# Performance work log

Hardware: AMD Instinct MI355X
Metric: run time of the kernel (lower is better)

## Reference

```python
import jax, jax.numpy as jnp
import numpy as np

HIDDEN_DIM = 2048
NUM_HEADS = 16
HEAD_DIM = HIDDEN_DIM // NUM_HEADS
BATCH = 2
SEQ = 2048


def setup_inputs() -> dict:
    key = jax.random.key(0)
    ks = jax.random.split(key, 5)
    scale = 1.0 / np.sqrt(HIDDEN_DIM)
    x = jax.random.normal(ks[0], (BATCH, SEQ, HIDDEN_DIM), dtype=jnp.float32)
    w_q = jax.random.normal(ks[1], (HIDDEN_DIM, HIDDEN_DIM), dtype=jnp.float32) * scale
    w_k = jax.random.normal(ks[2], (HIDDEN_DIM, HIDDEN_DIM), dtype=jnp.float32) * scale
    w_v = jax.random.normal(ks[3], (HIDDEN_DIM, HIDDEN_DIM), dtype=jnp.float32) * scale
    w_o = jax.random.normal(ks[4], (HIDDEN_DIM, HIDDEN_DIM), dtype=jnp.float32) * scale
    return {"x": x, "w_q": w_q, "w_k": w_k, "w_v": w_v, "w_o": w_o}


def reference(x, w_q, w_k, w_v, w_o):
    # Projections: x @ W.T  (weights stored as (out, in) like torch)
    q = jnp.einsum('bsd,ed->bse', x, w_q)
    k = jnp.einsum('bsd,ed->bse', x, w_k)
    v = jnp.einsum('bsd,ed->bse', x, w_v)
    b, s, _ = q.shape
    # split heads: (b, h, s, hd)
    q = q.reshape(b, s, NUM_HEADS, HEAD_DIM).transpose(0, 2, 1, 3)
    k = k.reshape(b, s, NUM_HEADS, HEAD_DIM).transpose(0, 2, 1, 3)
    v = v.reshape(b, s, NUM_HEADS, HEAD_DIM).transpose(0, 2, 1, 3)
    scale = 1.0 / np.sqrt(HEAD_DIM)
    # Online-softmax tiling in the source (causal=False default) is
    # mathematically identical to standard softmax attention.
    scores = jnp.einsum('bhqd,bhkd->bhqk', q, k) * scale
    p = jax.nn.softmax(scores, axis=-1)
    o = jnp.einsum('bhqk,bhkd->bhqd', p, v)
    o = o.transpose(0, 2, 1, 3).reshape(b, s, HIDDEN_DIM)
    return jnp.einsum('bsd,ed->bse', o, w_o)
```

## Files before the change

kernel.cpp:

```cpp
#include <hip/hip_runtime.h>


typedef _Float16 half8 __attribute__((ext_vector_type(8)));
typedef float floatx4 __attribute__((ext_vector_type(4)));

__device__ __forceinline__ void async16(const void* g, void* l) {
  __builtin_amdgcn_global_load_lds((__attribute__((address_space(1))) void*)(g),
                                   (__attribute__((address_space(3))) void*)(l),
                                   16, 0, 0);
}

__global__ void cvt_f32_f16(const float* __restrict__ src, _Float16* __restrict__ dst,
                            int n4) {
  int i = blockIdx.x * blockDim.x + threadIdx.x;
  if (i >= n4) return;
  float4 v = reinterpret_cast<const float4*>(src)[i];
  union { _Float16 h[4]; short4 s; } u;
  u.h[0] = (_Float16)v.x; u.h[1] = (_Float16)v.y;
  u.h[2] = (_Float16)v.z; u.h[3] = (_Float16)v.w;
  reinterpret_cast<short4*>(dst)[i] = u.s;
}

__global__ void cvt_w4(const float* __restrict__ w0, const float* __restrict__ w1,
                       const float* __restrict__ w2, const float* __restrict__ w3,
                       _Float16* __restrict__ dst, float scale0) {
  int i = blockIdx.x * blockDim.x + threadIdx.x;
  int m = i >> 20, j = i & ((1 << 20) - 1);
  const float* src = (m == 0) ? w0 : (m == 1) ? w1 : (m == 2) ? w2 : w3;
  float sc = (m == 0) ? scale0 : 1.0f;
  float4 v = reinterpret_cast<const float4*>(src)[j];
  union { _Float16 h[4]; short4 s; } u;
  u.h[0] = (_Float16)(v.x * sc); u.h[1] = (_Float16)(v.y * sc);
  u.h[2] = (_Float16)(v.z * sc); u.h[3] = (_Float16)(v.w * sc);
  reinterpret_cast<short4*>(dst)[i] = u.s;
}

template <int OUT_MODE, int BM, int BN, int MINW>
__global__ __launch_bounds__(256, MINW)
void gemm_nt(const _Float16* __restrict__ A, const _Float16* __restrict__ Bw,
             void* __restrict__ Cv, void* __restrict__ Cv2, int K) {
  constexpr int MT = BM / 32;
  constexpr int NT = BN / 32;
  __shared__ _Float16 As[BM * 64];
  __shared__ _Float16 Bs[BN * 64];
  const int tid = threadIdx.x;
  const int wave = tid >> 6, lane = tid & 63;
  const int wm = wave >> 1, wn = wave & 1;
  const int l15 = lane & 15, l4 = lane >> 4;
  const int bm = blockIdx.y, bn = blockIdx.x;

  floatx4 acc[MT][NT] = {};

  for (int k0 = 0; k0 < K; k0 += 64) {
    __syncthreads();
#pragma unroll
    for (int i = 0; i < BM * 8 / 256; ++i) {
      int c = i * 256 + tid;
      int row = c >> 3, cc = c & 7;
      int g = cc ^ (row & 7);
      async16(A + (size_t)(bm * BM + row) * K + k0 + g * 8, &As[c * 8]);
    }
#pragma unroll
    for (int i = 0; i < BN * 8 / 256; ++i) {
      int c = i * 256 + tid;
      int row = c >> 3, cc = c & 7;
      int g = cc ^ (row & 7);
      async16(Bw + (size_t)(bn * BN + row) * K + k0 + g * 8, &Bs[c * 8]);
    }
    __syncthreads();
#pragma unroll
    for (int ks = 0; ks < 2; ++ks) {
      half8 af[MT], bf[NT];
      int ch = (ks * 4 + l4) ^ (l15 & 7);
#pragma unroll
      for (int t = 0; t < MT; ++t)
        af[t] = *reinterpret_cast<const half8*>(&As[(wm * (BM / 2) + t * 16 + l15) * 64 + ch * 8]);
#pragma unroll
      for (int t = 0; t < NT; ++t)
        bf[t] = *reinterpret_cast<const half8*>(&Bs[(wn * (BN / 2) + t * 16 + l15) * 64 + ch * 8]);
#pragma unroll
      for (int mt = 0; mt < MT; ++mt)
#pragma unroll
        for (int nt = 0; nt < NT; ++nt)
          acc[mt][nt] = __builtin_amdgcn_mfma_f32_16x16x32_f16(af[mt], bf[nt], acc[mt][nt], 0, 0, 0);
    }
  }

  const int rbase = bm * BM + wm * (BM / 2);
  const int cbase = bn * BN + wn * (BN / 2);
  if constexpr (OUT_MODE == 0) {
    if (cbase < 4096) {
      _Float16* C = (_Float16*)Cv + (size_t)(cbase >> 11) * (4096ull * 2048);
#pragma unroll
      for (int mt = 0; mt < MT; ++mt)
#pragma unroll
        for (int nt = 0; nt < NT; ++nt) {
          int r0 = rbase + mt * 16 + l4 * 4;
          int cg = (cbase + nt * 16 + l15) & 2047;
#pragma unroll
          for (int r = 0; r < 4; ++r)
            C[(size_t)(r0 + r) * 2048 + cg] = (_Float16)acc[mt][nt][r];
        }
    } else {
      _Float16* C = (_Float16*)Cv2;
#pragma unroll
      for (int mt = 0; mt < MT; ++mt)
#pragma unroll
        for (int nt = 0; nt < NT; ++nt) {
          int m0 = rbase + mt * 16 + l4 * 4;
          int d = cbase + nt * 16 + l15 - 4096;
          size_t base = (size_t)(m0 >> 11) * (2048ull * 2048) + (size_t)d * 2048 + (m0 & 2047);
          union { _Float16 h[4]; short4 s; } u;
#pragma unroll
          for (int r = 0; r < 4; ++r) u.h[r] = (_Float16)acc[mt][nt][r];
          *reinterpret_cast<short4*>(C + base) = u.s;
        }
    }
  } else {
    float* C = (float*)Cv;
#pragma unroll
    for (int mt = 0; mt < MT; ++mt)
#pragma unroll
      for (int nt = 0; nt < NT; ++nt) {
        int r0 = rbase + mt * 16 + l4 * 4;
        int cg = cbase + nt * 16 + l15;
#pragma unroll
        for (int r = 0; r < 4; ++r)
          C[(size_t)(r0 + r) * 2048 + cg] = acc[mt][nt][r];
      }
  }
}

__global__ __launch_bounds__(256, 2)
void flash_attn(const _Float16* __restrict__ Q, const _Float16* __restrict__ Kg,
                const _Float16* __restrict__ Vt, _Float16* __restrict__ O) {
  __shared__ _Float16 Ks[64 * 128];
  __shared__ _Float16 Vs[128 * 64];
  __shared__ _Float16 Ps[128 * 64];
  const int tid = threadIdx.x, wave = tid >> 6, lane = tid & 63;
  const int l15 = lane & 15, l4 = lane >> 4;
  const int bh = blockIdx.y, b = bh >> 4, h = bh & 15;
  const int q0 = blockIdx.x * 128;

  const _Float16* Qp = Q + ((size_t)(b * 2048 + q0 + wave * 32)) * 2048 + h * 128;
  const _Float16* Kp = Kg + (size_t)b * 2048 * 2048 + h * 128;
  const _Float16* Vp = Vt + (size_t)b * 2048 * 2048 + (size_t)(h * 128) * 2048;

  half8 qf[2][4];
#pragma unroll
  for (int mt = 0; mt < 2; ++mt)
#pragma unroll
    for (int ks = 0; ks < 4; ++ks)
      qf[mt][ks] = *reinterpret_cast<const half8*>(
          Qp + (size_t)(mt * 16 + l15) * 2048 + ks * 32 + l4 * 8);

  floatx4 oacc[2][8] = {};
  float lsum[2][4] = {};

  for (int k0 = 0; k0 < 2048; k0 += 64) {
    __syncthreads();
#pragma unroll
    for (int i = 0; i < 4; ++i) {
      int c = i * 256 + tid;
      int row = c >> 4, cc = c & 15;
      int g = cc ^ (row & 15);
      async16(Kp + (size_t)(k0 + row) * 2048 + g * 8, &Ks[c * 8]);
    }
#pragma unroll
    for (int i = 0; i < 4; ++i) {
      int c = i * 256 + tid;
      int row = c >> 3, cc = c & 7;
      int g = cc ^ (row & 7);
      async16(Vp + (size_t)row * 2048 + k0 + g * 8, &Vs[c * 8]);
    }
    __syncthreads();

    floatx4 sacc[2][4] = {};
#pragma unroll
    for (int ks = 0; ks < 4; ++ks) {
      half8 bf[4];
#pragma unroll
      for (int nt = 0; nt < 4; ++nt) {
        int row = nt * 16 + l15;
        int ch = (ks * 4 + l4) ^ l15;
        bf[nt] = *reinterpret_cast<const half8*>(&Ks[row * 128 + ch * 8]);
      }
#pragma unroll
      for (int mt = 0; mt < 2; ++mt)
#pragma unroll
        for (int nt = 0; nt < 4; ++nt)
          sacc[mt][nt] = __builtin_amdgcn_mfma_f32_16x16x32_f16(qf[mt][ks], bf[nt], sacc[mt][nt], 0, 0, 0);
    }

#pragma unroll
    for (int mt = 0; mt < 2; ++mt)
#pragma unroll
      for (int nt = 0; nt < 4; ++nt)
#pragma unroll
        for (int r = 0; r < 4; ++r) {
          float p = exp2f(sacc[mt][nt][r]);
          lsum[mt][r] += p;
          int rl = l4 * 4 + r;
          int ch = (nt * 2 + (l15 >> 3)) ^ (rl & 7);
          Ps[(wave * 32 + mt * 16 + rl) * 64 + ch * 8 + (l15 & 7)] = (_Float16)p;
        }

    __builtin_amdgcn_s_waitcnt(0xC07F);

#pragma unroll
    for (int ks2 = 0; ks2 < 2; ++ks2) {
      half8 pf[2];
#pragma unroll
      for (int mt = 0; mt < 2; ++mt)
        pf[mt] = *reinterpret_cast<const half8*>(
            &Ps[(wave * 32 + mt * 16 + l15) * 64 + (((ks2 * 4 + l4) ^ (l15 & 7)) * 8)]);
#pragma unroll
      for (int nt2 = 0; nt2 < 8; ++nt2) {
        int row = nt2 * 16 + l15;
        int ch = (ks2 * 4 + l4) ^ (row & 7);
        half8 vf = *reinterpret_cast<const half8*>(&Vs[row * 64 + ch * 8]);
#pragma unroll
        for (int mt = 0; mt < 2; ++mt)
          oacc[mt][nt2] = __builtin_amdgcn_mfma_f32_16x16x32_f16(pf[mt], vf, oacc[mt][nt2], 0, 0, 0);
      }
    }
  }

#pragma unroll
  for (int mt = 0; mt < 2; ++mt)
#pragma unroll
    for (int r = 0; r < 4; ++r) {
#pragma unroll
      for (int off = 1; off < 16; off <<= 1) lsum[mt][r] += __shfl_xor(lsum[mt][r], off);
    }

  _Float16* Op = O + ((size_t)(b * 2048 + q0 + wave * 32)) * 2048 + h * 128;
#pragma unroll
  for (int mt = 0; mt < 2; ++mt)
#pragma unroll
    for (int r = 0; r < 4; ++r) {
      float inv = 1.0f / lsum[mt][r];
#pragma unroll
      for (int nt2 = 0; nt2 < 8; ++nt2) {
        int row = mt * 16 + l4 * 4 + r;
        int col = nt2 * 16 + l15;
        Op[(size_t)row * 2048 + col] = (_Float16)(oacc[mt][nt2][r] * inv);
      }
    }
}

extern "C" void kernel_launch(void* const* d_in, const int* in_sizes, int n_in,
                              void* d_out, int out_size, void* d_ws, size_t ws_size,
                              hipStream_t stream) {
  const float* x = (const float*)d_in[0];
  const float* wq = (const float*)d_in[1];
  const float* wk = (const float*)d_in[2];
  const float* wv = (const float*)d_in[3];
  const float* wo = (const float*)d_in[4];
  float* out = (float*)d_out;

  const size_t XN = (size_t)4096 * 2048;
  const size_t WN = (size_t)2048 * 2048;
  _Float16* xh = (_Float16*)d_ws;
  _Float16* qh = xh + XN;
  _Float16* vth = xh + 3 * XN;
  _Float16* oh = xh + 4 * XN;
  _Float16* wqh = xh + 5 * XN;

  const float SM_SCALE = 0.08838834764831845f * 1.4426950408889634f;

  cvt_f32_f16<<<dim3((int)(XN / 4 / 256)), 256, 0, stream>>>(x, xh, (int)(XN / 4));
  cvt_w4<<<dim3((int)(4 * WN / 4 / 256)), 256, 0, stream>>>(wq, wk, wv, wo, wqh, SM_SCALE);

  gemm_nt<0, 128, 128, 1><<<dim3(48, 32), 256, 0, stream>>>(xh, wqh, qh, vth, 2048);
  flash_attn<<<dim3(16, 32), 256, 0, stream>>>(qh, qh + XN, vth, oh);
  gemm_nt<2, 128, 64, 4><<<dim3(32, 32), 256, 0, stream>>>(oh, wqh + 3 * WN, out, nullptr, 2048);
}
```

Before: 406.2 us.

## Split-K the output projection with a reduction pass and fuse conversion kernels

The output projection GEMM switches from 128x64 tiles over the full K to 128x128 tiles with split-K of two. Each half writes fp32 partials into the workspace, where the earlier intermediates are now dead, and a new reduce_add kernel sums the two halves into the output. The two fp32-to-fp16 conversion kernels are merged into one launch, and the GEMM template is fixed to 128x128 tiles. The aim is a bigger per-wave MFMA tile and one fewer launch, at the cost of writing and re-reading large fp32 partial buffers plus an extra kernel launch.

```diff
diff --git a/kernel.cpp b/kernel.cpp
--- a/kernel.cpp
+++ b/kernel.cpp
@@ -10,91 +10,84 @@
                                    16, 0, 0);
 }
 
-__global__ void cvt_f32_f16(const float* __restrict__ src, _Float16* __restrict__ dst,
-                            int n4) {
+__global__ void cvt_all(const float* __restrict__ x, const float* __restrict__ w0,
+                        const float* __restrict__ w1, const float* __restrict__ w2,
+                        const float* __restrict__ w3, _Float16* __restrict__ xh,
+                        _Float16* __restrict__ wh, float scale0) {
   int i = blockIdx.x * blockDim.x + threadIdx.x;
-  if (i >= n4) return;
-  float4 v = reinterpret_cast<const float4*>(src)[i];
-  union { _Float16 h[4]; short4 s; } u;
-  u.h[0] = (_Float16)v.x; u.h[1] = (_Float16)v.y;
-  u.h[2] = (_Float16)v.z; u.h[3] = (_Float16)v.w;
-  reinterpret_cast<short4*>(dst)[i] = u.s;
-}
-
-__global__ void cvt_w4(const float* __restrict__ w0, const float* __restrict__ w1,
-                       const float* __restrict__ w2, const float* __restrict__ w3,
-                       _Float16* __restrict__ dst, float scale0) {
-  int i = blockIdx.x * blockDim.x + threadIdx.x;
-  int m = i >> 20, j = i & ((1 << 20) - 1);
-  const float* src = (m == 0) ? w0 : (m == 1) ? w1 : (m == 2) ? w2 : w3;
-  float sc = (m == 0) ? scale0 : 1.0f;
-  float4 v = reinterpret_cast<const float4*>(src)[j];
+  const int XQ = 1 << 21;
+  float sc = 1.0f;
+  const float* src;
+  _Float16* dst;
+  int j;
+  if (i < XQ) { src = x; dst = xh; j = i; }
+  else {
+    int t = i - XQ;
+    int m = t >> 20;
+    src = (m == 0) ? w0 : (m == 1) ? w1 : (m == 2) ? w2 : w3;
+    if (m == 0) sc = scale0;
+    dst = wh; j = t;
+  }
+  int js = (i < XQ) ? j : (j & ((1 << 20) - 1));
+  float4 v = reinterpret_cast<const float4*>(src)[js];
   union { _Float16 h[4]; short4 s; } u;
   u.h[0] = (_Float16)(v.x * sc); u.h[1] = (_Float16)(v.y * sc);
   u.h[2] = (_Float16)(v.z * sc); u.h[3] = (_Float16)(v.w * sc);
-  reinterpret_cast<short4*>(dst)[i] = u.s;
-}
-
-template <int OUT_MODE, int BM, int BN, int MINW>
-__global__ __launch_bounds__(256, MINW)
+  reinterpret_cast<short4*>(dst)[j] = u.s;
+}
+
+template <int OUT_MODE>
+__global__ __launch_bounds__(256)
 void gemm_nt(const _Float16* __restrict__ A, const _Float16* __restrict__ Bw,
-             void* __restrict__ Cv, void* __restrict__ Cv2, int K) {
-  constexpr int MT = BM / 32;
-  constexpr int NT = BN / 32;
-  __shared__ _Float16 As[BM * 64];
-  __shared__ _Float16 Bs[BN * 64];
+             void* __restrict__ Cv, void* __restrict__ Cv2, int kLen) {
+  __shared__ _Float16 As[128 * 64];
+  __shared__ _Float16 Bs[128 * 64];
   const int tid = threadIdx.x;
   const int wave = tid >> 6, lane = tid & 63;
   const int wm = wave >> 1, wn = wave & 1;
   const int l15 = lane & 15, l4 = lane >> 4;
   const int bm = blockIdx.y, bn = blockIdx.x;
-
-  floatx4 acc[MT][NT] = {};
-
-  for (int k0 = 0; k0 < K; k0 += 64) {
-    __syncthreads();
-#pragma unroll
-    for (int i = 0; i < BM * 8 / 256; ++i) {
+  const int kStart = (OUT_MODE == 2) ? blockIdx.z * kLen : 0;
+
+  floatx4 acc[4][4] = {};
+
+  for (int k0 = kStart; k0 < kStart + kLen; k0 += 64) {
+    __syncthreads();
+#pragma unroll
+    for (int i = 0; i < 4; ++i) {
       int c = i * 256 + tid;
       int row = c >> 3, cc = c & 7;
       int g = cc ^ (row & 7);
-      async16(A + (size_t)(bm * BM + row) * K + k0 + g * 8, &As[c * 8]);
-    }
-#pragma unroll
-    for (int i = 0; i < BN * 8 / 256; ++i) {
-      int c = i * 256 + tid;
-      int row = c >> 3, cc = c & 7;
-      int g = cc ^ (row & 7);
-      async16(Bw + (size_t)(bn * BN + row) * K + k0 + g * 8, &Bs[c * 8]);
+      async16(A + (size_t)(bm * 128 + row) * 2048 + k0 + g * 8, &As[c * 8]);
+      async16(Bw + (size_t)(bn * 128 + row) * 2048 + k0 + g * 8, &Bs[c * 8]);
     }
     __syncthreads();
 #pragma unroll
     for (int ks = 0; ks < 2; ++ks) {
-      half8 af[MT], bf[NT];
+      half8 af[4], bf[4];
       int ch = (ks * 4 + l4) ^ (l15 & 7);
 #pragma unroll
-      for (int t = 0; t < MT; ++t)
-        af[t] = *reinterpret_cast<const half8*>(&As[(wm * (BM / 2) + t * 16 + l15) * 64 + ch * 8]);
-#pragma unroll
-      for (int t = 0; t < NT; ++t)
-        bf[t] = *reinterpret_cast<const half8*>(&Bs[(wn * (BN / 2) + t * 16 + l15) * 64 + ch * 8]);
-#pragma unroll
-      for (int mt = 0; mt < MT; ++mt)
-#pragma unroll
-        for (int nt = 0; nt < NT; ++nt)
+      for (int t = 0; t < 4; ++t) {
+        af[t] = *reinterpret_cast<const half8*>(&As[(wm * 64 + t * 16 + l15) * 64 + ch * 8]);
+        bf[t] = *reinterpret_cast<const half8*>(&Bs[(wn * 64 + t * 16 + l15) * 64 + ch * 8]);
+      }
+#pragma unroll
+      for (int mt = 0; mt < 4; ++mt)
+#pragma unroll
+        for (int nt = 0; nt < 4; ++nt)
           acc[mt][nt] = __builtin_amdgcn_mfma_f32_16x16x32_f16(af[mt], bf[nt], acc[mt][nt], 0, 0, 0);
     }
   }
 
-  const int rbase = bm * BM + wm * (BM / 2);
-  const int cbase = bn * BN + wn * (BN / 2);
+  const int rbase = bm * 128 + wm * 64;
+  const int cbase = bn * 128 + wn * 64;
   if constexpr (OUT_MODE == 0) {
     if (cbase < 4096) {
       _Float16* C = (_Float16*)Cv + (size_t)(cbase >> 11) * (4096ull * 2048);
 #pragma unroll
-      for (int mt = 0; mt < MT; ++mt)
-#pragma unroll
-        for (int nt = 0; nt < NT; ++nt) {
+      for (int mt = 0; mt < 4; ++mt)
+#pragma unroll
+        for (int nt = 0; nt < 4; ++nt) {
           int r0 = rbase + mt * 16 + l4 * 4;
           int cg = (cbase + nt * 16 + l15) & 2047;
 #pragma unroll
@@ -104,9 +97,9 @@
     } else {
       _Float16* C = (_Float16*)Cv2;
 #pragma unroll
-      for (int mt = 0; mt < MT; ++mt)
-#pragma unroll
-        for (int nt = 0; nt < NT; ++nt) {
+      for (int mt = 0; mt < 4; ++mt)
+#pragma unroll
+        for (int nt = 0; nt < 4; ++nt) {
           int m0 = rbase + mt * 16 + l4 * 4;
           int d = cbase + nt * 16 + l15 - 4096;
           size_t base = (size_t)(m0 >> 11) * (2048ull * 2048) + (size_t)d * 2048 + (m0 & 2047);
@@ -117,11 +110,11 @@
         }
     }
   } else {
-    float* C = (float*)Cv;
-#pragma unroll
-    for (int mt = 0; mt < MT; ++mt)
-#pragma unroll
-      for (int nt = 0; nt < NT; ++nt) {
+    float* C = (float*)Cv + (size_t)blockIdx.z * 8388608ull;
+#pragma unroll
+    for (int mt = 0; mt < 4; ++mt)
+#pragma unroll
+      for (int nt = 0; nt < 4; ++nt) {
         int r0 = rbase + mt * 16 + l4 * 4;
         int cg = cbase + nt * 16 + l15;
 #pragma unroll
@@ -129,6 +122,14 @@
           C[(size_t)(r0 + r) * 2048 + cg] = acc[mt][nt][r];
       }
   }
+}
+
+__global__ void reduce_add(const float* __restrict__ p, float* __restrict__ out) {
+  int i = blockIdx.x * blockDim.x + threadIdx.x;
+  float4 a = reinterpret_cast<const float4*>(p)[i];
+  float4 b = reinterpret_cast<const float4*>(p + 8388608)[i];
+  float4 o; o.x = a.x + b.x; o.y = a.y + b.y; o.z = a.z + b.z; o.w = a.w + b.w;
+  reinterpret_cast<float4*>(out)[i] = o;
 }
 
 __global__ __launch_bounds__(256, 2)
@@ -266,13 +267,13 @@
   _Float16* vth = xh + 3 * XN;
   _Float16* oh = xh + 4 * XN;
   _Float16* wqh = xh + 5 * XN;
+  float* pparts = (float*)d_ws;
 
   const float SM_SCALE = 0.08838834764831845f * 1.4426950408889634f;
 
-  cvt_f32_f16<<<dim3((int)(XN / 4 / 256)), 256, 0, stream>>>(x, xh, (int)(XN / 4));
-  cvt_w4<<<dim3((int)(4 * WN / 4 / 256)), 256, 0, stream>>>(wq, wk, wv, wo, wqh, SM_SCALE);
-
-  gemm_nt<0, 128, 128, 1><<<dim3(48, 32), 256, 0, stream>>>(xh, wqh, qh, vth, 2048);
+  cvt_all<<<dim3(24576), 256, 0, stream>>>(x, wq, wk, wv, wo, xh, wqh, SM_SCALE);
+  gemm_nt<0><<<dim3(48, 32), 256, 0, stream>>>(xh, wqh, qh, vth, 2048);
   flash_attn<<<dim3(16, 32), 256, 0, stream>>>(qh, qh + XN, vth, oh);
-  gemm_nt<2, 128, 64, 4><<<dim3(32, 32), 256, 0, stream>>>(oh, wqh + 3 * WN, out, nullptr, 2048);
-}
+  gemm_nt<2><<<dim3(16, 32, 2), 256, 0, stream>>>(oh, wqh + 3 * WN, pparts, nullptr, 1024);
+  reduce_add<<<dim3(8192), 256, 0, stream>>>(pparts, out);
+}
```

After: 424.2 us. 1.04x slower.
